# Performance work log

Measured on AMD Instinct MI355X. Metric: run time of the kernel, lower is better.

## Reference

```python
import jax, jax.numpy as jnp
import numpy as np

DIM = 180
HEADS = 6
WH, WW = 8, 8
N = WH * WW
B_ = 4096
NW = 4096  # num windows per image; B_ // NW == 1


def _relative_position_index():
    coords = np.stack(np.meshgrid(np.arange(WH), np.arange(WW), indexing='ij'))  # (2,Wh,Ww)
    cf = coords.reshape(2, -1)                       # (2,N)
    rel = (cf[:, :, None] - cf[:, None, :]).transpose(1, 2, 0)  # (N,N,2)
    rel[:, :, 0] += WH - 1
    rel[:, :, 1] += WW - 1
    rel[:, :, 0] *= 2 * WW - 1
    return rel.sum(-1)                               # (N,N) int


def setup_inputs() -> dict:
    key = jax.random.key(0)
    ks = jax.random.split(key, 16)
    f32 = jnp.float32
    table_rows = (2 * WH - 1) * (2 * WW - 1)  # 225
    inp = {
        'e': jax.random.normal(ks[0], (B_, N, DIM), f32),
        'b': jax.random.normal(ks[1], (B_, N, DIM), f32),
        'mask': jax.random.normal(ks[2], (NW, N, N), f32),
        'rpb_table': 0.02 * jax.random.normal(ks[3], (table_rows, HEADS), f32),
        'rpi': jnp.asarray(_relative_position_index(), jnp.int32),
        # Linear weights stored as (in, out)
        'Wqkv_e': 0.02 * jax.random.normal(ks[4], (DIM, 3 * DIM), f32),
        'bqkv_e': jnp.zeros((3 * DIM,), f32),
        'Wqkv_b': 0.02 * jax.random.normal(ks[5], (DIM, 3 * DIM), f32),
        'bqkv_b': jnp.zeros((3 * DIM,), f32),
        'Wpe_s': 0.02 * jax.random.normal(ks[6], (DIM, DIM), f32),
        'bpe_s': jnp.zeros((DIM,), f32),
        'Wpb_s': 0.02 * jax.random.normal(ks[7], (DIM, DIM), f32),
        'bpb_s': jnp.zeros((DIM,), f32),
        'Wpe': 0.02 * jax.random.normal(ks[8], (2 * DIM, DIM), f32),
        'bpe': jnp.zeros((DIM,), f32),
        'Wpb': 0.02 * jax.random.normal(ks[9], (2 * DIM, DIM), f32),
        'bpb': jnp.zeros((DIM,), f32),
    }
    return inp


def _branch_attn(x, Wqkv, bqkv, bias, mask):
    Bw, n, C = x.shape
    hd = C // HEADS
    scale = hd ** -0.5
    qkv = (x @ Wqkv + bqkv).reshape(Bw, n, 3, HEADS, hd)
    q, k, v = (qkv[:, :, i].transpose(0, 2, 1, 3) for i in range(3))  # (Bw,H,n,hd)
    attn = jnp.einsum('bhnd,bhmd->bhnm', q * scale, k)
    attn = attn + bias[None]  # (Bw,H,n,n) + (1,H,n,n)
    # mask add: view as (Bw//NW, NW, H, n, n) + (1, NW, 1, n, n)
    attn = (attn.reshape(Bw // NW, NW, HEADS, n, n) + mask[None, :, None]).reshape(Bw, HEADS, n, n)
    attn = jax.nn.softmax(attn, axis=-1)
    out = jnp.einsum('bhnm,bhmd->bhnd', attn, v)
    return out.transpose(0, 2, 1, 3).reshape(Bw, n, C)


def reference(e, b, mask, rpb_table, rpi, Wqkv_e, bqkv_e, Wqkv_b, bqkv_b,
              Wpe_s, bpe_s, Wpb_s, bpb_s, Wpe, bpe, Wpb, bpb):
    e_sig = jax.nn.sigmoid(e @ Wpe_s + bpe_s)
    b_sig = jax.nn.sigmoid(b @ Wpb_s + bpb_s)
    bias = rpb_table[rpi].transpose(2, 0, 1)  # (H,N,N)
    out_e = _branch_attn(e, Wqkv_e, bqkv_e, bias, mask)
    out_b = _branch_attn(b, Wqkv_b, bqkv_b, bias, mask)
    out_1 = jnp.concatenate([out_e * e_sig, out_b * e_sig], -1) @ Wpe + bpe
    out_2 = jnp.concatenate([out_e * b_sig, out_b * b_sig], -1) @ Wpb + bpb
    return (out_1, out_2)
```

## Files before the change

kernel.cpp:

```cpp
#include <hip/hip_runtime.h>

#define DIMC 180
#define NHEADS 6
#define NTOK 64
#define NWIN 4096
#define OUT1_ELEMS (NWIN * NTOK * DIMC)

typedef _Float16 f16;
typedef _Float16 f16x8 __attribute__((ext_vector_type(8)));
typedef _Float16 f16x4 __attribute__((ext_vector_type(4)));
typedef float    f32x4 __attribute__((ext_vector_type(4)));

#define WS_WQKV_E   0
#define WS_WQKV_B   221184
#define WS_WPS_E    442368
#define WS_WPS_B    516096
#define WS_WPE_T    589824
#define WS_WPB_T    737280
#define WS_BQKV_E   884736
#define WS_BQKV_B   887040
#define WS_BPS_E    889344
#define WS_BPS_B    890112
#define WS_BIAS     890880


__global__ __launch_bounds__(256) void pack_kernel(
    const float* __restrict__ Wqkv_e, const float* __restrict__ bqkv_e,
    const float* __restrict__ Wqkv_b, const float* __restrict__ bqkv_b,
    const float* __restrict__ Wpe_s,  const float* __restrict__ bpe_s,
    const float* __restrict__ Wpb_s,  const float* __restrict__ bpb_s,
    const float* __restrict__ Wpe,    const float* __restrict__ Wpb,
    const float* __restrict__ rpb_table, const int* __restrict__ rpi,
    unsigned char* __restrict__ ws)
{
    const int gid  = blockIdx.x * blockDim.x + threadIdx.x;
    const int nthr = gridDim.x * blockDim.x;

    f16* wq = (f16*)(ws + WS_WQKV_E);
    for (int idx = gid; idx < 2 * 576 * 192; idx += nthr) {
        int br = idx / (576 * 192), r = idx % (576 * 192);
        int c = r / 192, k = r % 192;
        int s = c / 192, rr = c % 192, h = rr / 32, d = rr % 32;
        const float* W = br ? Wqkv_b : Wqkv_e;
        float v = (d < 30 && k < 180) ? W[k * 540 + s * 180 + h * 30 + d] : 0.f;
        wq[idx] = (f16)v;
    }
    f16* wp = (f16*)(ws + WS_WPS_E);
    for (int idx = gid; idx < 2 * 192 * 192; idx += nthr) {
        int br = idx / (192 * 192), r = idx % (192 * 192);
        int c = r / 192, k = r % 192;
        const float* W = br ? Wpb_s : Wpe_s;
        float v = (c < 180 && k < 180) ? W[k * 180 + c] : 0.f;
        wp[idx] = (f16)v;
    }
    f16* wt = (f16*)(ws + WS_WPE_T);
    for (int idx = gid; idx < 2 * 192 * 384; idx += nthr) {
        int o = idx / (192 * 384), r = idx % (192 * 384);
        int c = r / 384, k = r % 384;
        const float* W = o ? Wpb : Wpe;
        int krow = (k < 180) ? k : ((k >= 192 && k < 372) ? (180 + k - 192) : -1);
        float v = (c < 180 && krow >= 0) ? W[krow * 180 + c] : 0.f;
        wt[idx] = (f16)v;
    }
    float* bq = (float*)(ws + WS_BQKV_E);
    for (int idx = gid; idx < 2 * 576; idx += nthr) {
        int br = idx / 576, c = idx % 576;
        int s = c / 192, rr = c % 192, h = rr / 32, d = rr % 32;
        const float* B = br ? bqkv_b : bqkv_e;
        bq[idx] = (d < 30) ? B[s * 180 + h * 30 + d] : 0.f;
    }
    float* bp = (float*)(ws + WS_BPS_E);
    for (int idx = gid; idx < 2 * 192; idx += nthr) {
        int br = idx / 192, c = idx % 192;
        const float* B = br ? bpb_s : bpe_s;
        bp[idx] = (c < 180) ? B[c] : 0.f;
    }
    float* bh = (float*)(ws + WS_BIAS);
    for (int idx = gid; idx < 6 * 4096; idx += nthr) {
        int h = idx / 4096, ij = idx % 4096;
        bh[idx] = rpb_table[rpi[ij] * NHEADS + h];
    }
}

__global__ __launch_bounds__(256) void attn_kernel(
    const float* __restrict__ e, const float* __restrict__ b,
    const float* __restrict__ mask,
    const unsigned char* __restrict__ ws,
    float* __restrict__ d_out)
{
    const int w    = blockIdx.x;
    const int br   = blockIdx.y;
    const int tid  = threadIdx.x;
    const int lane = tid & 63;
    const int l15  = lane & 15;
    const int l4   = lane >> 4;
    const int wid  = __builtin_amdgcn_readfirstlane(tid >> 6);

    __shared__ f16 sX[64 * 200];
    __shared__ f16 sQ[64 * 40];
    __shared__ f16 sK[64 * 40];
    __shared__ f16 sVt[32 * 72];
    __shared__ f16 sP[64 * 72];

    const float* x   = br ? b : e;
    const f16*   Wq  = (const f16*)(ws + (br ? WS_WQKV_B : WS_WQKV_E));
    const f16*   Wp  = (const f16*)(ws + (br ? WS_WPS_B  : WS_WPS_E));
    const float* bq  = (const float*)(ws + (br ? WS_BQKV_B : WS_BQKV_E));
    const float* bp  = (const float*)(ws + (br ? WS_BPS_B  : WS_BPS_E));
    const float* bh0 = (const float*)(ws + WS_BIAS);

    const float* xw = x + (size_t)w * (NTOK * DIMC);
    for (int idx = tid; idx < 2880; idx += 256) {
        int row = idx / 45, c4 = (idx % 45) * 4;
        const float4 v = *(const float4*)(xw + row * 180 + c4);
        f16x4 hv = { (f16)v.x, (f16)v.y, (f16)v.z, (f16)v.w };
        *(f16x4*)&sX[row * 200 + c4] = hv;
    }
    for (int idx = tid; idx < 320; idx += 256) {
        int row = idx / 5, c4 = 180 + (idx % 5) * 4;
        *(f16x4*)&sX[row * 200 + c4] = (f16x4){0, 0, 0, 0};
    }
    float mreg[4][4];
    {
        const float* mw = mask + (size_t)w * 4096;
        const int rbase = wid * 16 + l4 * 4;
#pragma unroll
        for (int nt = 0; nt < 4; ++nt)
#pragma unroll
            for (int r = 0; r < 4; ++r)
                mreg[nt][r] = mw[(rbase + r) * 64 + nt * 16 + l15];
    }
    __syncthreads();

    f16x8 a[6];
#pragma unroll
    for (int kk = 0; kk < 6; ++kk)
        a[kk] = *(const f16x8*)&sX[(wid * 16 + l15) * 200 + kk * 32 + l4 * 8];

    f16* sig_stage = (f16*)d_out;
    {
        const size_t base = (size_t)w * 23040 + (size_t)br * 11520;
        for (int nt = 0; nt < 12; ++nt) {
            f32x4 acc = {0, 0, 0, 0};
#pragma unroll
            for (int kk = 0; kk < 6; ++kk) {
                f16x8 bf = *(const f16x8*)&Wp[(size_t)(nt * 16 + l15) * 192 + kk * 32 + l4 * 8];
                acc = __builtin_amdgcn_mfma_f32_16x16x32_f16(a[kk], bf, acc, 0, 0, 0);
            }
            const int col = nt * 16 + l15;
            if (col < 180) {
                const float bv = bp[col];
#pragma unroll
                for (int r = 0; r < 4; ++r) {
                    const int row = wid * 16 + l4 * 4 + r;
                    float s = 1.f / (1.f + __expf(-(acc[r] + bv)));
                    sig_stage[base + row * 180 + col] = (f16)s;
                }
            }
        }
    }

    f16* out_stage = (f16*)(d_out + OUT1_ELEMS);
    const float scale = 0.18257418583505536f;

    for (int h = 0; h < NHEADS; ++h) {
#pragma unroll
        for (int sec = 0; sec < 3; ++sec) {
#pragma unroll
            for (int nt = 0; nt < 2; ++nt) {
                const int colp = sec * 192 + h * 32 + nt * 16;
                f32x4 acc = {0, 0, 0, 0};
#pragma unroll
                for (int kk = 0; kk < 6; ++kk) {
                    f16x8 bf = *(const f16x8*)&Wq[(size_t)(colp + l15) * 192 + kk * 32 + l4 * 8];
                    acc = __builtin_amdgcn_mfma_f32_16x16x32_f16(a[kk], bf, acc, 0, 0, 0);
                }
                const float bv = bq[colp + l15];
                const int d = nt * 16 + l15;
                if (sec == 2) {
                    f16x4 vv;
#pragma unroll
                    for (int r = 0; r < 4; ++r) vv[r] = (f16)(acc[r] + bv);
                    *(f16x4*)&sVt[d * 72 + wid * 16 + l4 * 4] = vv;
                } else {
                    f16* dst = sec ? sK : sQ;
#pragma unroll
                    for (int r = 0; r < 4; ++r)
                        dst[(wid * 16 + l4 * 4 + r) * 40 + d] = (f16)(acc[r] + bv);
                }
            }
        }
        __syncthreads();

        const float* bh = bh0 + h * 4096;
        const f16x8 qa = *(const f16x8*)&sQ[(wid * 16 + l15) * 40 + l4 * 8];
        float sc[4][4];
#pragma unroll
        for (int nt = 0; nt < 4; ++nt) {
            f16x8 kb = *(const f16x8*)&sK[(nt * 16 + l15) * 40 + l4 * 8];
            f32x4 s4 = __builtin_amdgcn_mfma_f32_16x16x32_f16(qa, kb, (f32x4){0, 0, 0, 0}, 0, 0, 0);
            const int rbase = wid * 16 + l4 * 4;
            const int col = nt * 16 + l15;
#pragma unroll
            for (int r = 0; r < 4; ++r)
                sc[nt][r] = scale * s4[r] + bh[(rbase + r) * 64 + col] + mreg[nt][r];
        }
#pragma unroll
        for (int r = 0; r < 4; ++r) {
            float mx = fmaxf(fmaxf(sc[0][r], sc[1][r]), fmaxf(sc[2][r], sc[3][r]));
#pragma unroll
            for (int m = 8; m >= 1; m >>= 1) mx = fmaxf(mx, __shfl_xor(mx, m, 64));
            float p0 = __expf(sc[0][r] - mx);
            float p1 = __expf(sc[1][r] - mx);
            float p2 = __expf(sc[2][r] - mx);
            float p3 = __expf(sc[3][r] - mx);
            float sum = p0 + p1 + p2 + p3;
#pragma unroll
            for (int m = 8; m >= 1; m >>= 1) sum += __shfl_xor(sum, m, 64);
            const float inv = 1.f / sum;
            const int row = wid * 16 + l4 * 4 + r;
            sP[row * 72 +      l15] = (f16)(p0 * inv);
            sP[row * 72 + 16 + l15] = (f16)(p1 * inv);
            sP[row * 72 + 32 + l15] = (f16)(p2 * inv);
            sP[row * 72 + 48 + l15] = (f16)(p3 * inv);
        }
        const f16x8 pa0 = *(const f16x8*)&sP[(wid * 16 + l15) * 72 + l4 * 8];
        const f16x8 pa1 = *(const f16x8*)&sP[(wid * 16 + l15) * 72 + 32 + l4 * 8];
#pragma unroll
        for (int nt = 0; nt < 2; ++nt) {
            f32x4 oacc = {0, 0, 0, 0};
            f16x8 vb0 = *(const f16x8*)&sVt[(nt * 16 + l15) * 72 + l4 * 8];
            f16x8 vb1 = *(const f16x8*)&sVt[(nt * 16 + l15) * 72 + 32 + l4 * 8];
            oacc = __builtin_amdgcn_mfma_f32_16x16x32_f16(pa0, vb0, oacc, 0, 0, 0);
            oacc = __builtin_amdgcn_mfma_f32_16x16x32_f16(pa1, vb1, oacc, 0, 0, 0);
            const int d = nt * 16 + l15;
            if (d < 30) {
                const size_t obase = (size_t)w * 23040 + (size_t)br * 11520 + (size_t)(h * 30 + d);
#pragma unroll
                for (int r = 0; r < 4; ++r) {
                    const int row = wid * 16 + l4 * 4 + r;
                    out_stage[obase + (size_t)row * 180] = (f16)oacc[r];
                }
            }
        }
        __syncthreads();
    }
}

__global__ __launch_bounds__(512) void final_kernel(
    const float* __restrict__ bpe, const float* __restrict__ bpb,
    const unsigned char* __restrict__ ws, float* __restrict__ d_out)
{
    const int w    = blockIdx.x;
    const int tid  = threadIdx.x;
    const int lane = tid & 63;
    const int l15  = lane & 15;
    const int l4   = lane >> 4;
    const int wid  = __builtin_amdgcn_readfirstlane(tid >> 6);
    const int mt     = wid & 3;
    const int outsel = wid >> 2;

    __shared__ f16 sG1[64 * 200];
    __shared__ f16 sG2[64 * 200];

    const f16* o_stage = (const f16*)(d_out + OUT1_ELEMS);
    const f16* s_stage = (const f16*)d_out;
    const f16* Wt = (const f16*)(ws + (outsel ? WS_WPB_T : WS_WPE_T));

    for (int idx = tid; idx < 320; idx += 512) {
        int row = idx / 5, c4 = 180 + (idx % 5) * 4;
        *(f16x4*)&sG1[row * 200 + c4] = (f16x4){0, 0, 0, 0};
        *(f16x4*)&sG2[row * 200 + c4] = (f16x4){0, 0, 0, 0};
    }

    f32x4 acc[12];
#pragma unroll
    for (int nt = 0; nt < 12; ++nt) acc[nt] = (f32x4){0, 0, 0, 0};

    const size_t sbase = (size_t)w * 23040;
    for (int half = 0; half < 2; ++half) {
        __syncthreads();
        for (int idx = tid; idx < 2880; idx += 512) {
            int row = idx / 45, c4 = (idx % 45) * 4;
            f16x4 o4 = *(const f16x4*)&o_stage[sbase + half * 11520 + row * 180 + c4];
            f16x4 e4 = *(const f16x4*)&s_stage[sbase + row * 180 + c4];
            f16x4 b4 = *(const f16x4*)&s_stage[sbase + 11520 + row * 180 + c4];
            f16x4 g1, g2;
#pragma unroll
            for (int q = 0; q < 4; ++q) { g1[q] = o4[q] * e4[q]; g2[q] = o4[q] * b4[q]; }
            *(f16x4*)&sG1[row * 200 + c4] = g1;
            *(f16x4*)&sG2[row * 200 + c4] = g2;
        }
        __syncthreads();
        const f16* Gs = outsel ? sG2 : sG1;
        f16x8 a[6];
#pragma unroll
        for (int kk = 0; kk < 6; ++kk)
            a[kk] = *(const f16x8*)&Gs[(mt * 16 + l15) * 200 + kk * 32 + l4 * 8];
#pragma unroll
        for (int nt = 0; nt < 12; ++nt) {
#pragma unroll
            for (int kk = 0; kk < 6; ++kk) {
                f16x8 bf = *(const f16x8*)&Wt[(size_t)(nt * 16 + l15) * 384 + half * 192 + kk * 32 + l4 * 8];
                acc[nt] = __builtin_amdgcn_mfma_f32_16x16x32_f16(a[kk], bf, acc[nt], 0, 0, 0);
            }
        }
    }

    const float* bias = outsel ? bpb : bpe;
    float* dst = d_out + (outsel ? (size_t)OUT1_ELEMS : (size_t)0) + (size_t)w * 11520;
#pragma unroll
    for (int nt = 0; nt < 12; ++nt) {
        const int col = nt * 16 + l15;
        if (col < 180) {
            const float bv = bias[col];
#pragma unroll
            for (int r = 0; r < 4; ++r) {
                const int row = mt * 16 + l4 * 4 + r;
                dst[(size_t)row * 180 + col] = acc[nt][r] + bv;
            }
        }
    }
}

extern "C" void kernel_launch(void* const* d_in, const int* in_sizes, int n_in,
                              void* d_out, int out_size, void* d_ws, size_t ws_size,
                              hipStream_t stream) {
    const float* e      = (const float*)d_in[0];
    const float* b      = (const float*)d_in[1];
    const float* mask   = (const float*)d_in[2];
    const float* rpb    = (const float*)d_in[3];
    const int*   rpi    = (const int*)  d_in[4];
    const float* Wqkv_e = (const float*)d_in[5];
    const float* bqkv_e = (const float*)d_in[6];
    const float* Wqkv_b = (const float*)d_in[7];
    const float* bqkv_b = (const float*)d_in[8];
    const float* Wpe_s  = (const float*)d_in[9];
    const float* bpe_s  = (const float*)d_in[10];
    const float* Wpb_s  = (const float*)d_in[11];
    const float* bpb_s  = (const float*)d_in[12];
    const float* Wpe    = (const float*)d_in[13];
    const float* bpe    = (const float*)d_in[14];
    const float* Wpb    = (const float*)d_in[15];
    const float* bpb    = (const float*)d_in[16];
    float* out = (float*)d_out;
    unsigned char* ws = (unsigned char*)d_ws;

    pack_kernel<<<dim3(128), dim3(256), 0, stream>>>(
        Wqkv_e, bqkv_e, Wqkv_b, bqkv_b, Wpe_s, bpe_s, Wpb_s, bpb_s,
        Wpe, Wpb, rpb, rpi, ws);
    attn_kernel<<<dim3(NWIN, 2), dim3(256), 0, stream>>>(e, b, mask, ws, out);
    final_kernel<<<dim3(NWIN), dim3(512), 0, stream>>>(bpe, bpb, ws, out);
}
```

Baseline: 2.636 ms.

## Cut LDS footprint via buffer aliasing and K-chunking to raise occupancy

The attention kernel now places all shared buffers in one byte array and lets sQ alias sX. A barrier is added after the X fragments are loaded into registers so the overlap stays safe, and launch bounds ask for 6 blocks per CU. The final projection kernel stages the gated inputs in two 96-column chunks per half, which roughly halves its LDS, and requests 4 blocks per CU. The aim is more resident waves to hide memory latency, at the cost of extra barriers, more staging passes, and possible register spills from the tighter bounds.

```diff
diff --git a/kernel.cpp b/kernel.cpp
--- a/kernel.cpp
+++ b/kernel.cpp
@@ -82,7 +82,7 @@
     }
 }
 
-__global__ __launch_bounds__(256) void attn_kernel(
+__global__ __launch_bounds__(256, 6) void attn_kernel(
     const float* __restrict__ e, const float* __restrict__ b,
     const float* __restrict__ mask,
     const unsigned char* __restrict__ ws,
@@ -96,11 +96,12 @@
     const int l4   = lane >> 4;
     const int wid  = __builtin_amdgcn_readfirstlane(tid >> 6);
 
-    __shared__ f16 sX[64 * 200];
-    __shared__ f16 sQ[64 * 40];
-    __shared__ f16 sK[64 * 40];
-    __shared__ f16 sVt[32 * 72];
-    __shared__ f16 sP[64 * 72];
+    __shared__ __align__(16) unsigned char smem[25600];
+    f16* sX  = (f16*)smem;
+    f16* sQ  = (f16*)smem;
+    f16* sK  = (f16*)(smem + 5120);
+    f16* sVt = (f16*)(smem + 10240);
+    f16* sP  = (f16*)(smem + 14848);
 
     const float* x   = br ? b : e;
     const f16*   Wq  = (const f16*)(ws + (br ? WS_WQKV_B : WS_WQKV_E));
@@ -136,6 +137,7 @@
 #pragma unroll
     for (int kk = 0; kk < 6; ++kk)
         a[kk] = *(const f16x8*)&sX[(wid * 16 + l15) * 200 + kk * 32 + l4 * 8];
+    __syncthreads();
 
     f16* sig_stage = (f16*)d_out;
     {
@@ -247,7 +249,7 @@
     }
 }
 
-__global__ __launch_bounds__(512) void final_kernel(
+__global__ __launch_bounds__(512, 4) void final_kernel(
     const float* __restrict__ bpe, const float* __restrict__ bpb,
     const unsigned char* __restrict__ ws, float* __restrict__ d_out)
 {
@@ -260,49 +262,48 @@
     const int mt     = wid & 3;
     const int outsel = wid >> 2;
 
-    __shared__ f16 sG1[64 * 200];
-    __shared__ f16 sG2[64 * 200];
+    __shared__ f16 sG1[64 * 104];
+    __shared__ f16 sG2[64 * 104];
 
     const f16* o_stage = (const f16*)(d_out + OUT1_ELEMS);
     const f16* s_stage = (const f16*)d_out;
     const f16* Wt = (const f16*)(ws + (outsel ? WS_WPB_T : WS_WPE_T));
 
-    for (int idx = tid; idx < 320; idx += 512) {
-        int row = idx / 5, c4 = 180 + (idx % 5) * 4;
-        *(f16x4*)&sG1[row * 200 + c4] = (f16x4){0, 0, 0, 0};
-        *(f16x4*)&sG2[row * 200 + c4] = (f16x4){0, 0, 0, 0};
-    }
-
     f32x4 acc[12];
 #pragma unroll
     for (int nt = 0; nt < 12; ++nt) acc[nt] = (f32x4){0, 0, 0, 0};
 
     const size_t sbase = (size_t)w * 23040;
     for (int half = 0; half < 2; ++half) {
-        __syncthreads();
-        for (int idx = tid; idx < 2880; idx += 512) {
-            int row = idx / 45, c4 = (idx % 45) * 4;
-            f16x4 o4 = *(const f16x4*)&o_stage[sbase + half * 11520 + row * 180 + c4];
-            f16x4 e4 = *(const f16x4*)&s_stage[sbase + row * 180 + c4];
-            f16x4 b4 = *(const f16x4*)&s_stage[sbase + 11520 + row * 180 + c4];
-            f16x4 g1, g2;
-#pragma unroll
-            for (int q = 0; q < 4; ++q) { g1[q] = o4[q] * e4[q]; g2[q] = o4[q] * b4[q]; }
-            *(f16x4*)&sG1[row * 200 + c4] = g1;
-            *(f16x4*)&sG2[row * 200 + c4] = g2;
-        }
-        __syncthreads();
-        const f16* Gs = outsel ? sG2 : sG1;
-        f16x8 a[6];
-#pragma unroll
-        for (int kk = 0; kk < 6; ++kk)
-            a[kk] = *(const f16x8*)&Gs[(mt * 16 + l15) * 200 + kk * 32 + l4 * 8];
-#pragma unroll
-        for (int nt = 0; nt < 12; ++nt) {
-#pragma unroll
-            for (int kk = 0; kk < 6; ++kk) {
-                f16x8 bf = *(const f16x8*)&Wt[(size_t)(nt * 16 + l15) * 384 + half * 192 + kk * 32 + l4 * 8];
-                acc[nt] = __builtin_amdgcn_mfma_f32_16x16x32_f16(a[kk], bf, acc[nt], 0, 0, 0);
+        for (int ch = 0; ch < 2; ++ch) {
+            __syncthreads();
+            for (int idx = tid; idx < 1536; idx += 512) {
+                int row = idx / 24, c4i = (idx % 24) * 4;
+                int c = ch * 96 + c4i;
+                f16x4 g1 = {0, 0, 0, 0}, g2 = {0, 0, 0, 0};
+                if (c < 180) {
+                    f16x4 o4 = *(const f16x4*)&o_stage[sbase + half * 11520 + row * 180 + c];
+                    f16x4 e4 = *(const f16x4*)&s_stage[sbase + row * 180 + c];
+                    f16x4 b4 = *(const f16x4*)&s_stage[sbase + 11520 + row * 180 + c];
+#pragma unroll
+                    for (int q = 0; q < 4; ++q) { g1[q] = o4[q] * e4[q]; g2[q] = o4[q] * b4[q]; }
+                }
+                *(f16x4*)&sG1[row * 104 + c4i] = g1;
+                *(f16x4*)&sG2[row * 104 + c4i] = g2;
+            }
+            __syncthreads();
+            const f16* Gs = outsel ? sG2 : sG1;
+            f16x8 a[3];
+#pragma unroll
+            for (int kk = 0; kk < 3; ++kk)
+                a[kk] = *(const f16x8*)&Gs[(mt * 16 + l15) * 104 + kk * 32 + l4 * 8];
+#pragma unroll
+            for (int nt = 0; nt < 12; ++nt) {
+#pragma unroll
+                for (int kk = 0; kk < 3; ++kk) {
+                    f16x8 bf = *(const f16x8*)&Wt[(size_t)(nt * 16 + l15) * 384 + half * 192 + ch * 96 + kk * 32 + l4 * 8];
+                    acc[nt] = __builtin_amdgcn_mfma_f32_16x16x32_f16(a[kk], bf, acc[nt], 0, 0, 0);
+                }
             }
         }
     }
```

After: 2.719 ms. 3.1% more time.

## Fuse attention, gating and output projection into one per-window kernel

Applied to the files above, without the earlier changes.

Merges the attention kernel and the final projection kernel into a single 512-thread block per window. The two branches run in separate 4-wave groups, and each head's output is gated and multiplied into the final projection accumulators right away. This removes the fp16 staging round trip of attention outputs and sigmoid gates through global memory, and one kernel launch. The weights are repacked per head, which adds per-head barriers and heavier register use (12 accumulator tiles held across the head loop) and may lower occupancy.

```diff
diff --git a/kernel.cpp b/kernel.cpp
--- a/kernel.cpp
+++ b/kernel.cpp
@@ -15,8 +15,7 @@
 #define WS_WQKV_B   221184
 #define WS_WPS_E    442368
 #define WS_WPS_B    516096
-#define WS_WPE_T    589824
-#define WS_WPB_T    737280
+#define WS_WFIN     589824
 #define WS_BQKV_E   884736
 #define WS_BQKV_B   887040
 #define WS_BPS_E    889344
@@ -49,17 +48,19 @@
     for (int idx = gid; idx < 2 * 192 * 192; idx += nthr) {
         int br = idx / (192 * 192), r = idx % (192 * 192);
         int c = r / 192, k = r % 192;
+        int h = c / 32, d = c % 32;
         const float* W = br ? Wpb_s : Wpe_s;
-        float v = (c < 180 && k < 180) ? W[k * 180 + c] : 0.f;
+        float v = (d < 30 && k < 180) ? W[k * 180 + h * 30 + d] : 0.f;
         wp[idx] = (f16)v;
     }
-    f16* wt = (f16*)(ws + WS_WPE_T);
-    for (int idx = gid; idx < 2 * 192 * 384; idx += nthr) {
-        int o = idx / (192 * 384), r = idx % (192 * 384);
-        int c = r / 384, k = r % 384;
+    f16* wt = (f16*)(ws + WS_WFIN);
+    for (int idx = gid; idx < 2 * 2 * 6 * 192 * 32; idx += nthr) {
+        int o  = idx / 73728, r = idx % 73728;
+        int be = r / 36864;  r %= 36864;
+        int h  = r / 6144;   r %= 6144;
+        int col = r / 32, d = r % 32;
         const float* W = o ? Wpb : Wpe;
-        int krow = (k < 180) ? k : ((k >= 192 && k < 372) ? (180 + k - 192) : -1);
-        float v = (c < 180 && krow >= 0) ? W[krow * 180 + c] : 0.f;
+        float v = (col < 180 && d < 30) ? W[(be * 180 + h * 30 + d) * 180 + col] : 0.f;
         wt[idx] = (f16)v;
     }
     float* bq = (float*)(ws + WS_BQKV_E);
@@ -72,8 +73,9 @@
     float* bp = (float*)(ws + WS_BPS_E);
     for (int idx = gid; idx < 2 * 192; idx += nthr) {
         int br = idx / 192, c = idx % 192;
+        int h = c / 32, d = c % 32;
         const float* B = br ? bpb_s : bpe_s;
-        bp[idx] = (c < 180) ? B[c] : 0.f;
+        bp[idx] = (d < 30) ? B[h * 30 + d] : 0.f;
     }
     float* bh = (float*)(ws + WS_BIAS);
     for (int idx = gid; idx < 6 * 4096; idx += nthr) {
@@ -82,174 +84,12 @@
     }
 }
 
-__global__ __launch_bounds__(256) void attn_kernel(
+__global__ __launch_bounds__(512, 4) void fused_kernel(
     const float* __restrict__ e, const float* __restrict__ b,
     const float* __restrict__ mask,
     const unsigned char* __restrict__ ws,
+    const float* __restrict__ bpe, const float* __restrict__ bpb,
     float* __restrict__ d_out)
-{
-    const int w    = blockIdx.x;
-    const int br   = blockIdx.y;
-    const int tid  = threadIdx.x;
-    const int lane = tid & 63;
-    const int l15  = lane & 15;
-    const int l4   = lane >> 4;
-    const int wid  = __builtin_amdgcn_readfirstlane(tid >> 6);
-
-    __shared__ f16 sX[64 * 200];
-    __shared__ f16 sQ[64 * 40];
-    __shared__ f16 sK[64 * 40];
-    __shared__ f16 sVt[32 * 72];
-    __shared__ f16 sP[64 * 72];
-
-    const float* x   = br ? b : e;
-    const f16*   Wq  = (const f16*)(ws + (br ? WS_WQKV_B : WS_WQKV_E));
-    const f16*   Wp  = (const f16*)(ws + (br ? WS_WPS_B  : WS_WPS_E));
-    const float* bq  = (const float*)(ws + (br ? WS_BQKV_B : WS_BQKV_E));
-    const float* bp  = (const float*)(ws + (br ? WS_BPS_B  : WS_BPS_E));
-    const float* bh0 = (const float*)(ws + WS_BIAS);
-
-    const float* xw = x + (size_t)w * (NTOK * DIMC);
-    for (int idx = tid; idx < 2880; idx += 256) {
-        int row = idx / 45, c4 = (idx % 45) * 4;
-        const float4 v = *(const float4*)(xw + row * 180 + c4);
-        f16x4 hv = { (f16)v.x, (f16)v.y, (f16)v.z, (f16)v.w };
-        *(f16x4*)&sX[row * 200 + c4] = hv;
-    }
-    for (int idx = tid; idx < 320; idx += 256) {
-        int row = idx / 5, c4 = 180 + (idx % 5) * 4;
-        *(f16x4*)&sX[row * 200 + c4] = (f16x4){0, 0, 0, 0};
-    }
-    float mreg[4][4];
-    {
-        const float* mw = mask + (size_t)w * 4096;
-        const int rbase = wid * 16 + l4 * 4;
-#pragma unroll
-        for (int nt = 0; nt < 4; ++nt)
-#pragma unroll
-            for (int r = 0; r < 4; ++r)
-                mreg[nt][r] = mw[(rbase + r) * 64 + nt * 16 + l15];
-    }
-    __syncthreads();
-
-    f16x8 a[6];
-#pragma unroll
-    for (int kk = 0; kk < 6; ++kk)
-        a[kk] = *(const f16x8*)&sX[(wid * 16 + l15) * 200 + kk * 32 + l4 * 8];
-
-    f16* sig_stage = (f16*)d_out;
-    {
-        const size_t base = (size_t)w * 23040 + (size_t)br * 11520;
-        for (int nt = 0; nt < 12; ++nt) {
-            f32x4 acc = {0, 0, 0, 0};
-#pragma unroll
-            for (int kk = 0; kk < 6; ++kk) {
-                f16x8 bf = *(const f16x8*)&Wp[(size_t)(nt * 16 + l15) * 192 + kk * 32 + l4 * 8];
-                acc = __builtin_amdgcn_mfma_f32_16x16x32_f16(a[kk], bf, acc, 0, 0, 0);
-            }
-            const int col = nt * 16 + l15;
-            if (col < 180) {
-                const float bv = bp[col];
-#pragma unroll
-                for (int r = 0; r < 4; ++r) {
-                    const int row = wid * 16 + l4 * 4 + r;
-                    float s = 1.f / (1.f + __expf(-(acc[r] + bv)));
-                    sig_stage[base + row * 180 + col] = (f16)s;
-                }
-            }
-        }
-    }
-
-    f16* out_stage = (f16*)(d_out + OUT1_ELEMS);
-    const float scale = 0.18257418583505536f;
-
-    for (int h = 0; h < NHEADS; ++h) {
-#pragma unroll
-        for (int sec = 0; sec < 3; ++sec) {
-#pragma unroll
-            for (int nt = 0; nt < 2; ++nt) {
-                const int colp = sec * 192 + h * 32 + nt * 16;
-                f32x4 acc = {0, 0, 0, 0};
-#pragma unroll
-                for (int kk = 0; kk < 6; ++kk) {
-                    f16x8 bf = *(const f16x8*)&Wq[(size_t)(colp + l15) * 192 + kk * 32 + l4 * 8];
-                    acc = __builtin_amdgcn_mfma_f32_16x16x32_f16(a[kk], bf, acc, 0, 0, 0);
-                }
-                const float bv = bq[colp + l15];
-                const int d = nt * 16 + l15;
-                if (sec == 2) {
-                    f16x4 vv;
-#pragma unroll
-                    for (int r = 0; r < 4; ++r) vv[r] = (f16)(acc[r] + bv);
-                    *(f16x4*)&sVt[d * 72 + wid * 16 + l4 * 4] = vv;
-                } else {
-                    f16* dst = sec ? sK : sQ;
-#pragma unroll
-                    for (int r = 0; r < 4; ++r)
-                        dst[(wid * 16 + l4 * 4 + r) * 40 + d] = (f16)(acc[r] + bv);
-                }
-            }
-        }
-        __syncthreads();
-
-        const float* bh = bh0 + h * 4096;
-        const f16x8 qa = *(const f16x8*)&sQ[(wid * 16 + l15) * 40 + l4 * 8];
-        float sc[4][4];
-#pragma unroll
-        for (int nt = 0; nt < 4; ++nt) {
-            f16x8 kb = *(const f16x8*)&sK[(nt * 16 + l15) * 40 + l4 * 8];
-            f32x4 s4 = __builtin_amdgcn_mfma_f32_16x16x32_f16(qa, kb, (f32x4){0, 0, 0, 0}, 0, 0, 0);
-            const int rbase = wid * 16 + l4 * 4;
-            const int col = nt * 16 + l15;
-#pragma unroll
-            for (int r = 0; r < 4; ++r)
-                sc[nt][r] = scale * s4[r] + bh[(rbase + r) * 64 + col] + mreg[nt][r];
-        }
-#pragma unroll
-        for (int r = 0; r < 4; ++r) {
-            float mx = fmaxf(fmaxf(sc[0][r], sc[1][r]), fmaxf(sc[2][r], sc[3][r]));
-#pragma unroll
-            for (int m = 8; m >= 1; m >>= 1) mx = fmaxf(mx, __shfl_xor(mx, m, 64));
-            float p0 = __expf(sc[0][r] - mx);
-            float p1 = __expf(sc[1][r] - mx);
-            float p2 = __expf(sc[2][r] - mx);
-            float p3 = __expf(sc[3][r] - mx);
-            float sum = p0 + p1 + p2 + p3;
-#pragma unroll
-            for (int m = 8; m >= 1; m >>= 1) sum += __shfl_xor(sum, m, 64);
-            const float inv = 1.f / sum;
-            const int row = wid * 16 + l4 * 4 + r;
-            sP[row * 72 +      l15] = (f16)(p0 * inv);
-            sP[row * 72 + 16 + l15] = (f16)(p1 * inv);
-            sP[row * 72 + 32 + l15] = (f16)(p2 * inv);
-            sP[row * 72 + 48 + l15] = (f16)(p3 * inv);
-        }
-        const f16x8 pa0 = *(const f16x8*)&sP[(wid * 16 + l15) * 72 + l4 * 8];
-        const f16x8 pa1 = *(const f16x8*)&sP[(wid * 16 + l15) * 72 + 32 + l4 * 8];
-#pragma unroll
-        for (int nt = 0; nt < 2; ++nt) {
-            f32x4 oacc = {0, 0, 0, 0};
-            f16x8 vb0 = *(const f16x8*)&sVt[(nt * 16 + l15) * 72 + l4 * 8];
-            f16x8 vb1 = *(const f16x8*)&sVt[(nt * 16 + l15) * 72 + 32 + l4 * 8];
-            oacc = __builtin_amdgcn_mfma_f32_16x16x32_f16(pa0, vb0, oacc, 0, 0, 0);
-            oacc = __builtin_amdgcn_mfma_f32_16x16x32_f16(pa1, vb1, oacc, 0, 0, 0);
-            const int d = nt * 16 + l15;
-            if (d < 30) {
-                const size_t obase = (size_t)w * 23040 + (size_t)br * 11520 + (size_t)(h * 30 + d);
-#pragma unroll
-                for (int r = 0; r < 4; ++r) {
-                    const int row = wid * 16 + l4 * 4 + r;
-                    out_stage[obase + (size_t)row * 180] = (f16)oacc[r];
-                }
-            }
-        }
-        __syncthreads();
-    }
-}
-
-__global__ __launch_bounds__(512) void final_kernel(
-    const float* __restrict__ bpe, const float* __restrict__ bpb,
-    const unsigned char* __restrict__ ws, float* __restrict__ d_out)
 {
     const int w    = blockIdx.x;
     const int tid  = threadIdx.x;
@@ -257,58 +97,176 @@
     const int l15  = lane & 15;
     const int l4   = lane >> 4;
     const int wid  = __builtin_amdgcn_readfirstlane(tid >> 6);
-    const int mt     = wid & 3;
-    const int outsel = wid >> 2;
-
-    __shared__ f16 sG1[64 * 200];
-    __shared__ f16 sG2[64 * 200];
-
-    const f16* o_stage = (const f16*)(d_out + OUT1_ELEMS);
-    const f16* s_stage = (const f16*)d_out;
-    const f16* Wt = (const f16*)(ws + (outsel ? WS_WPB_T : WS_WPE_T));
-
-    for (int idx = tid; idx < 320; idx += 512) {
-        int row = idx / 5, c4 = 180 + (idx % 5) * 4;
-        *(f16x4*)&sG1[row * 200 + c4] = (f16x4){0, 0, 0, 0};
-        *(f16x4*)&sG2[row * 200 + c4] = (f16x4){0, 0, 0, 0};
-    }
+    const int mt   = wid & 3;
+    const int g    = wid >> 2;
+
+    __shared__ __align__(16) unsigned char smem[71680];
+    f16* sXg   = (f16*)(smem + g * 25600);
+    f16* sQg   = (f16*)(smem + g * 25600);
+    f16* sKg   = (f16*)(smem + g * 25600 + 5120);
+    f16* sVtg  = (f16*)(smem + g * 25600 + 10240);
+    f16* sPg   = (f16*)(smem + g * 25600 + 14848);
+    f16* sO0   = (f16*)(smem + 51200);
+    f16* sO1   = (f16*)(smem + 56320);
+    f16* sOg   = (f16*)(smem + 51200 + g * 5120);
+    f16* sGateg= (f16*)(smem + 61440 + g * 5120);
+
+    const f16*   Wq  = (const f16*)(ws + (g ? WS_WQKV_B : WS_WQKV_E));
+    const f16*   Wp  = (const f16*)(ws + (g ? WS_WPS_B  : WS_WPS_E));
+    const f16*   Wfin= (const f16*)(ws + WS_WFIN);
+    const float* bq  = (const float*)(ws + (g ? WS_BQKV_B : WS_BQKV_E));
+    const float* bp  = (const float*)(ws + (g ? WS_BPS_B  : WS_BPS_E));
+    const float* bh0 = (const float*)(ws + WS_BIAS);
+
+    for (int idx = tid; idx < 2 * 2880; idx += 512) {
+        int which = idx / 2880, r = idx % 2880;
+        int row = r / 45, c4 = (r % 45) * 4;
+        const float* src = (which ? b : e) + (size_t)w * 11520;
+        const float4 v = *(const float4*)(src + row * 180 + c4);
+        f16x4 hv = { (f16)v.x, (f16)v.y, (f16)v.z, (f16)v.w };
+        *(f16x4*)((f16*)(smem + which * 25600) + row * 200 + c4) = hv;
+    }
+    for (int idx = tid; idx < 2 * 320; idx += 512) {
+        int which = idx / 320, r = idx % 320;
+        int row = r / 5, c4 = 180 + (r % 5) * 4;
+        *(f16x4*)((f16*)(smem + which * 25600) + row * 200 + c4) = (f16x4){0, 0, 0, 0};
+    }
+    float mreg[4][4];
+    {
+        const float* mw = mask + (size_t)w * 4096;
+        const int rbase = mt * 16 + l4 * 4;
+#pragma unroll
+        for (int nt = 0; nt < 4; ++nt)
+#pragma unroll
+            for (int r = 0; r < 4; ++r)
+                mreg[nt][r] = mw[(rbase + r) * 64 + nt * 16 + l15];
+    }
+    __syncthreads();
+
+    f16x8 a[6];
+#pragma unroll
+    for (int kk = 0; kk < 6; ++kk)
+        a[kk] = *(const f16x8*)&sXg[(mt * 16 + l15) * 200 + kk * 32 + l4 * 8];
+    __syncthreads();
 
     f32x4 acc[12];
 #pragma unroll
     for (int nt = 0; nt < 12; ++nt) acc[nt] = (f32x4){0, 0, 0, 0};
 
-    const size_t sbase = (size_t)w * 23040;
-    for (int half = 0; half < 2; ++half) {
+    const float scale = 0.18257418583505536f;
+
+    for (int h = 0; h < NHEADS; ++h) {
+#pragma unroll
+        for (int sec = 0; sec < 3; ++sec) {
+#pragma unroll
+            for (int nt = 0; nt < 2; ++nt) {
+                const int colp = sec * 192 + h * 32 + nt * 16;
+                f32x4 qacc = {0, 0, 0, 0};
+#pragma unroll
+                for (int kk = 0; kk < 6; ++kk) {
+                    f16x8 bf = *(const f16x8*)&Wq[(size_t)(colp + l15) * 192 + kk * 32 + l4 * 8];
+                    qacc = __builtin_amdgcn_mfma_f32_16x16x32_f16(a[kk], bf, qacc, 0, 0, 0);
+                }
+                const float bv = bq[colp + l15];
+                const int d = nt * 16 + l15;
+                if (sec == 2) {
+                    f16x4 vv;
+#pragma unroll
+                    for (int r = 0; r < 4; ++r) vv[r] = (f16)(qacc[r] + bv);
+                    *(f16x4*)&sVtg[d * 72 + mt * 16 + l4 * 4] = vv;
+                } else {
+                    f16* dst = sec ? sKg : sQg;
+#pragma unroll
+                    for (int r = 0; r < 4; ++r)
+                        dst[(mt * 16 + l4 * 4 + r) * 40 + d] = (f16)(qacc[r] + bv);
+                }
+            }
+        }
+#pragma unroll
+        for (int nt = 0; nt < 2; ++nt) {
+            const int colp = h * 32 + nt * 16;
+            f32x4 gacc = {0, 0, 0, 0};
+#pragma unroll
+            for (int kk = 0; kk < 6; ++kk) {
+                f16x8 bf = *(const f16x8*)&Wp[(size_t)(colp + l15) * 192 + kk * 32 + l4 * 8];
+                gacc = __builtin_amdgcn_mfma_f32_16x16x32_f16(a[kk], bf, gacc, 0, 0, 0);
+            }
+            const float bv = bp[colp + l15];
+            const int d = nt * 16 + l15;
+#pragma unroll
+            for (int r = 0; r < 4; ++r) {
+                float s = 1.f / (1.f + __expf(-(gacc[r] + bv)));
+                sGateg[(mt * 16 + l4 * 4 + r) * 40 + d] = (f16)s;
+            }
+        }
         __syncthreads();
-        for (int idx = tid; idx < 2880; idx += 512) {
-            int row = idx / 45, c4 = (idx % 45) * 4;
-            f16x4 o4 = *(const f16x4*)&o_stage[sbase + half * 11520 + row * 180 + c4];
-            f16x4 e4 = *(const f16x4*)&s_stage[sbase + row * 180 + c4];
-            f16x4 b4 = *(const f16x4*)&s_stage[sbase + 11520 + row * 180 + c4];
-            f16x4 g1, g2;
-#pragma unroll
-            for (int q = 0; q < 4; ++q) { g1[q] = o4[q] * e4[q]; g2[q] = o4[q] * b4[q]; }
-            *(f16x4*)&sG1[row * 200 + c4] = g1;
-            *(f16x4*)&sG2[row * 200 + c4] = g2;
+
+        const float* bh = bh0 + h * 4096;
+        const f16x8 qa = *(const f16x8*)&sQg[(mt * 16 + l15) * 40 + l4 * 8];
+        float sc[4][4];
+#pragma unroll
+        for (int nt = 0; nt < 4; ++nt) {
+            f16x8 kb = *(const f16x8*)&sKg[(nt * 16 + l15) * 40 + l4 * 8];
+            f32x4 s4 = __builtin_amdgcn_mfma_f32_16x16x32_f16(qa, kb, (f32x4){0, 0, 0, 0}, 0, 0, 0);
+            const int rbase = mt * 16 + l4 * 4;
+            const int col = nt * 16 + l15;
+#pragma unroll
+            for (int r = 0; r < 4; ++r)
+                sc[nt][r] = scale * s4[r] + bh[(rbase + r) * 64 + col] + mreg[nt][r];
+        }
+#pragma unroll
+        for (int r = 0; r < 4; ++r) {
+            float mx = fmaxf(fmaxf(sc[0][r], sc[1][r]), fmaxf(sc[2][r], sc[3][r]));
+#pragma unroll
+            for (int m = 8; m >= 1; m >>= 1) mx = fmaxf(mx, __shfl_xor(mx, m, 64));
+            float p0 = __expf(sc[0][r] - mx);
+            float p1 = __expf(sc[1][r] - mx);
+            float p2 = __expf(sc[2][r] - mx);
+            float p3 = __expf(sc[3][r] - mx);
+            float sum = p0 + p1 + p2 + p3;
+#pragma unroll
+            for (int m = 8; m >= 1; m >>= 1) sum += __shfl_xor(sum, m, 64);
+            const float inv = 1.f / sum;
+            const int row = mt * 16 + l4 * 4 + r;
+            sPg[row * 72 +      l15] = (f16)(p0 * inv);
+            sPg[row * 72 + 16 + l15] = (f16)(p1 * inv);
+            sPg[row * 72 + 32 + l15] = (f16)(p2 * inv);
+            sPg[row * 72 + 48 + l15] = (f16)(p3 * inv);
+        }
+        const f16x8 pa0 = *(const f16x8*)&sPg[(mt * 16 + l15) * 72 + l4 * 8];
+        const f16x8 pa1 = *(const f16x8*)&sPg[(mt * 16 + l15) * 72 + 32 + l4 * 8];
+#pragma unroll
+        for (int nt = 0; nt < 2; ++nt) {
+            f32x4 oacc = {0, 0, 0, 0};
+            f16x8 vb0 = *(const f16x8*)&sVtg[(nt * 16 + l15) * 72 + l4 * 8];
+            f16x8 vb1 = *(const f16x8*)&sVtg[(nt * 16 + l15) * 72 + 32 + l4 * 8];
+            oacc = __builtin_amdgcn_mfma_f32_16x16x32_f16(pa0, vb0, oacc, 0, 0, 0);
+            oacc = __builtin_amdgcn_mfma_f32_16x16x32_f16(pa1, vb1, oacc, 0, 0, 0);
+            const int d = nt * 16 + l15;
+#pragma unroll
+            for (int r = 0; r < 4; ++r)
+                sOg[(mt * 16 + l4 * 4 + r) * 40 + d] = (f16)oacc[r];
         }
         __syncthreads();
-        const f16* Gs = outsel ? sG2 : sG1;
-        f16x8 a[6];
-#pragma unroll
-        for (int kk = 0; kk < 6; ++kk)
-            a[kk] = *(const f16x8*)&Gs[(mt * 16 + l15) * 200 + kk * 32 + l4 * 8];
-#pragma unroll
-        for (int nt = 0; nt < 12; ++nt) {
-#pragma unroll
-            for (int kk = 0; kk < 6; ++kk) {
-                f16x8 bf = *(const f16x8*)&Wt[(size_t)(nt * 16 + l15) * 384 + half * 192 + kk * 32 + l4 * 8];
-                acc[nt] = __builtin_amdgcn_mfma_f32_16x16x32_f16(a[kk], bf, acc[nt], 0, 0, 0);
-            }
-        }
-    }
-
-    const float* bias = outsel ? bpb : bpe;
-    float* dst = d_out + (outsel ? (size_t)OUT1_ELEMS : (size_t)0) + (size_t)w * 11520;
+
+#pragma unroll
+        for (int be = 0; be < 2; ++be) {
+            const f16* sOb = be ? sO1 : sO0;
+            f16x8 ov = *(const f16x8*)&sOb[(mt * 16 + l15) * 40 + l4 * 8];
+            f16x8 gv = *(const f16x8*)&sGateg[(mt * 16 + l15) * 40 + l4 * 8];
+            f16x8 Af = ov * gv;
+            const f16* wb = Wfin + (size_t)((g * 2 + be) * 6 + h) * 6144;
+#pragma unroll
+            for (int nt = 0; nt < 12; ++nt) {
+                f16x8 bf = *(const f16x8*)&wb[(nt * 16 + l15) * 32 + l4 * 8];
+                acc[nt] = __builtin_amdgcn_mfma_f32_16x16x32_f16(Af, bf, acc[nt], 0, 0, 0);
+            }
+        }
+        __syncthreads();
+    }
+
+    const float* bias = g ? bpb : bpe;
+    float* dst = d_out + (g ? (size_t)OUT1_ELEMS : (size_t)0) + (size_t)w * 11520;
 #pragma unroll
     for (int nt = 0; nt < 12; ++nt) {
         const int col = nt * 16 + l15;
@@ -349,6 +307,6 @@
     pack_kernel<<<dim3(128), dim3(256), 0, stream>>>(
         Wqkv_e, bqkv_e, Wqkv_b, bqkv_b, Wpe_s, bpe_s, Wpb_s, bpb_s,
         Wpe, Wpb, rpb, rpi, ws);
-    attn_kernel<<<dim3(NWIN, 2), dim3(256), 0, stream>>>(e, b, mask, ws, out);
-    final_kernel<<<dim3(NWIN), dim3(512), 0, stream>>>(bpe, bpb, ws, out);
+    fused_kernel<<<dim3(NWIN), dim3(512), 0, stream>>>(
+        e, b, mask, ws, bpe, bpb, out);
 }
```

After: 2.602 ms. Within noise of the previous version (-1.3%).
